# Optimization experiments

Measured on AMD Instinct MI355X. Metric: run time of the kernel, lower is better.

## Reference

```python
import jax, jax.numpy as jnp
import numpy as np

EPS_NORM = 1e-9   # l2_norm eps in original
EPS_ENT = 1e-15   # PyG dense_diff_pool entropy eps


def _sage_block(x, adj, Wl, bl, Wr):
    """SAGEConv(aggr='mean') + ReLU + row L2-norm.
    x: [b,N,din], adj: [b,N,N] binary (adj[i,j]=1 means edge i->j).
    PyG mean-aggr for target j = mean over sources i: (A^T x)/max(deg_in,1).
    out = lin_l(aggr) + lin_r(x); lin_l has bias, lin_r does not.
    """
    deg = jnp.sum(adj, axis=1)                                  # [b,N] in-degree of targets
    agg = jnp.einsum('bij,bid->bjd', adj, x) / jnp.maximum(deg, 1.0)[..., None]
    h = jnp.einsum('bnd,od->bno', agg, Wl) + bl + jnp.einsum('bnd,od->bno', x, Wr)
    h = jax.nn.relu(h)
    return h / (jnp.linalg.norm(h, axis=-1, keepdims=True) + EPS_NORM)


def setup_inputs() -> dict:
    key = jax.random.key(0)
    ks = jax.random.split(key, 16)
    b, N, din, dh, K = 8, 2048, 128, 128, 128
    x = jax.random.normal(ks[0], (b, N, din), dtype=jnp.float32)
    # binary adjacency, avg in-degree ~ 0.01*N ~ 20
    adj = (jax.random.uniform(ks[1], (b, N, N)) < 0.01).astype(jnp.float32)

    def lin(k, o, i):
        return (jax.random.normal(k, (o, i), dtype=jnp.float32) / np.sqrt(i)).astype(jnp.float32)

    return {
        'x': x, 'adj': adj,
        'We1l': lin(ks[2], dh, din), 'be1': jnp.zeros((dh,), jnp.float32), 'We1r': lin(ks[3], dh, din),
        'We2l': lin(ks[4], dh, dh),  'be2': jnp.zeros((dh,), jnp.float32), 'We2r': lin(ks[5], dh, dh),
        'Wa1l': lin(ks[6], dh, din), 'ba1': jnp.zeros((dh,), jnp.float32), 'Wa1r': lin(ks[7], dh, din),
        'Wa2l': lin(ks[8], K, dh),   'ba2': jnp.zeros((K,), jnp.float32), 'Wa2r': lin(ks[9], K, dh),
    }


def reference(x, adj, We1l, be1, We1r, We2l, be2, We2r, Wa1l, ba1, Wa1r, Wa2l, ba2, Wa2r):
    # embedding GNN
    h = _sage_block(x, adj, We1l, be1, We1r)
    h_emb = _sage_block(h, adj, We2l, be2, We2r)          # [b,N,dh]
    # assignment GNN
    a = _sage_block(x, adj, Wa1l, ba1, Wa1r)
    a = _sage_block(a, adj, Wa2l, ba2, Wa2r)              # [b,N,K]
    S = jax.nn.softmax(a, axis=-1)                        # [b,N,K]
    # dense_diff_pool
    h_pooled = jnp.einsum('bnk,bnd->bkd', S, h_emb)       # [b,K,dh]
    adj_pooled = jnp.einsum('bnk,bnm,bml->bkl', S, adj, S)  # [b,K,K]
    link = adj - jnp.einsum('bnk,bmk->bnm', S, S)
    link_loss = jnp.linalg.norm(link) / adj.size          # global Frobenius / numel
    ent_loss = jnp.mean(jnp.sum(-S * jnp.log(S + EPS_ENT), axis=-1))
    return h_pooled, adj_pooled, link_loss, ent_loss
```

## Files before the change

### kernel.cpp

```cpp
#include <hip/hip_runtime.h>
#include <hip/hip_bf16.h>
#include <math.h>

#define BB 8
#define NN 2048
#define DD 128
#define SPL 8
#define CAPH 16

typedef __bf16 bf16x8 __attribute__((ext_vector_type(8)));
typedef float f32x4 __attribute__((ext_vector_type(4)));

__device__ inline unsigned short f2bu(float f) {
  __hip_bfloat16 h = __float2bfloat16(f);
  return *reinterpret_cast<unsigned short*>(&h);
}
__device__ inline unsigned int pack2(float a, float b) {
  return (unsigned int)f2bu(a) | ((unsigned int)f2bu(b) << 16);
}
__device__ inline float blo(unsigned u) { return __uint_as_float(u << 16); }
__device__ inline float bhi(unsigned u) { return __uint_as_float(u & 0xffff0000u); }

__global__ __launch_bounds__(256) void k_build(const float* __restrict__ adj,
                                               const float* __restrict__ x,
                                               unsigned short* __restrict__ colidx,
                                               float* __restrict__ cnth,
                                               float* __restrict__ nnzpart,
                                               __hip_bfloat16* __restrict__ xb) {
  __shared__ float T[2][64][65];
  __shared__ unsigned short L[64][4][CAPH];
  __shared__ int cnts[64][4];
  __shared__ float tsum[64];
  int b = blockIdx.y, j0 = blockIdx.x * 64, z = blockIdx.z;
  int linear = (z * 8 + blockIdx.y) * 32 + blockIdx.x;
  const float* A = adj + (size_t)b * NN * NN + (size_t)z * 1024 * NN + j0;
  int t = threadIdx.x;
  int lr = t >> 2, lc0 = (t & 3) * 16;
  int sc = t & 63, sq = t >> 6;
  float4 pre[4];
  #pragma unroll
  for (int e = 0; e < 4; ++e)
    pre[e] = *(const float4*)(A + (size_t)lr * NN + lc0 + e * 4);
  #pragma unroll
  for (int e = 0; e < 4; ++e)
    *(float4*)&T[0][lr][lc0 + e * 4] = pre[e];
  __syncthreads();
  int cnt = 0;
  for (int ch = 0; ch < 16; ++ch) {
    if (ch + 1 < 16) {
      const float* src = A + (size_t)(ch + 1) * 64 * NN;
      #pragma unroll
      for (int e = 0; e < 4; ++e)
        pre[e] = *(const float4*)(src + (size_t)lr * NN + lc0 + e * 4);
    }
    #pragma unroll
    for (int p = 0; p < 16; ++p) {
      int il = sq * 16 + p;
      float v = T[ch & 1][il][sc];
      if (v != 0.f) {
        L[sc][sq][cnt < CAPH ? cnt : CAPH - 1] = (unsigned short)(z * 1024 + ch * 64 + il);
        ++cnt;
      }
    }
    if (ch + 1 < 16) {
      #pragma unroll
      for (int e = 0; e < 4; ++e)
        *(float4*)&T[(ch + 1) & 1][lr][lc0 + e * 4] = pre[e];
    }
    __syncthreads();
  }
  cnts[sc][sq] = cnt;
  __syncthreads();
  int c = t >> 2, seg = t & 3;
  int n0 = cnts[c][0], n1 = cnts[c][1], n2 = cnts[c][2], n3 = cnts[c][3];
  int tot = n0 + n1 + n2 + n3;
  unsigned short vals[8];
  #pragma unroll
  for (int e = 0; e < 8; ++e) {
    int k = seg * 8 + e;
    unsigned short xv = 0;
    if (k < n0) xv = L[c][0][k];
    else if (k < n0 + n1) xv = L[c][1][k - n0];
    else if (k < n0 + n1 + n2) xv = L[c][2][k - n0 - n1];
    else if (k < tot) xv = L[c][3][k - n0 - n1 - n2];
    vals[e] = xv;
  }
  size_t jg = (size_t)b * NN + j0 + c;
  *(uint4*)(colidx + jg * 64 + z * 32 + seg * 8) = *(uint4*)vals;
  if (seg == 0) {
    cnth[(size_t)z * (BB * NN) + jg] = (float)tot;
    tsum[c] = (float)tot;
  }
  __syncthreads();
  if (t < 64) {
    float s = tsum[t];
    #pragma unroll
    for (int off = 32; off > 0; off >>= 1) s += __shfl_xor(s, off);
    if (t == 0) nnzpart[linear] = s;
  }
  if (z == 0) {
    size_t base = (size_t)(blockIdx.y * 32 + blockIdx.x) * 8192;
    #pragma unroll
    for (int e = 0; e < 8; ++e) {
      size_t off = base + e * 1024 + t * 4;
      float4 a = *(const float4*)(x + off);
      unsigned r2[2] = {pack2(a.x, a.y), pack2(a.z, a.w)};
      *(uint2*)((unsigned short*)xb + off) = *(uint2*)r2;
    }
  }
}

__global__ __launch_bounds__(256) void k_agg(const __hip_bfloat16* __restrict__ V,
                                             const unsigned short* __restrict__ colidx,
                                             const float* __restrict__ cnth,
                                             __hip_bfloat16* __restrict__ out) {
  int w = threadIdx.x >> 6, l = threadIdx.x & 63;
  size_t jg = (size_t)blockIdx.x * 4 + w;
  int b = (int)(jg >> 11);
  int c0 = min((int)cnth[jg], 32);
  int c1 = min((int)cnth[(size_t)BB * NN + jg], 32);
  float sc = 1.f / fmaxf((float)(c0 + c1), 1.f);
  int myi = colidx[jg * 64 + l];
  const unsigned short* Vb = (const unsigned short*)V + (((size_t)b << 11)) * DD;
  float ax = 0.f, ay = 0.f;
  #pragma unroll
  for (int sgm = 0; sgm < 2; ++sgm) {
    int cc = sgm ? c1 : c0;
    int lb = sgm ? 32 : 0;
    int k = 0;
    for (; k + 4 <= cc; k += 4) {
      int i0 = __shfl(myi, lb + k), i1 = __shfl(myi, lb + k + 1);
      int i2 = __shfl(myi, lb + k + 2), i3 = __shfl(myi, lb + k + 3);
      unsigned u0 = *(const unsigned*)(Vb + (size_t)i0 * DD + 2 * l);
      unsigned u1 = *(const unsigned*)(Vb + (size_t)i1 * DD + 2 * l);
      unsigned u2 = *(const unsigned*)(Vb + (size_t)i2 * DD + 2 * l);
      unsigned u3 = *(const unsigned*)(Vb + (size_t)i3 * DD + 2 * l);
      ax += blo(u0) + blo(u1) + blo(u2) + blo(u3);
      ay += bhi(u0) + bhi(u1) + bhi(u2) + bhi(u3);
    }
    for (; k < cc; ++k) {
      int i0 = __shfl(myi, lb + k);
      unsigned u0 = *(const unsigned*)(Vb + (size_t)i0 * DD + 2 * l);
      ax += blo(u0); ay += bhi(u0);
    }
  }
  *(unsigned*)((unsigned short*)out + jg * DD + 2 * l) = pack2(ax * sc, ay * sc);
}

__global__ __launch_bounds__(256) void k_agg2(const __hip_bfloat16* __restrict__ V1,
                                              const __hip_bfloat16* __restrict__ V2,
                                              const unsigned short* __restrict__ colidx,
                                              const float* __restrict__ cnth,
                                              __hip_bfloat16* __restrict__ out1,
                                              __hip_bfloat16* __restrict__ out2) {
  int w = threadIdx.x >> 6, l = threadIdx.x & 63;
  size_t jg = (size_t)blockIdx.x * 4 + w;
  int b = (int)(jg >> 11);
  int c0 = min((int)cnth[jg], 32);
  int c1 = min((int)cnth[(size_t)BB * NN + jg], 32);
  float sc = 1.f / fmaxf((float)(c0 + c1), 1.f);
  int myi = colidx[jg * 64 + l];
  size_t base = (((size_t)b << 11)) * DD + 2 * l;
  const unsigned short* Va = (const unsigned short*)V1 + base;
  const unsigned short* Vb = (const unsigned short*)V2 + base;
  float ax = 0.f, ay = 0.f, bx = 0.f, by = 0.f;
  #pragma unroll
  for (int sgm = 0; sgm < 2; ++sgm) {
    int cc = sgm ? c1 : c0;
    int lb = sgm ? 32 : 0;
    int k = 0;
    for (; k + 2 <= cc; k += 2) {
      int i0 = __shfl(myi, lb + k), i1 = __shfl(myi, lb + k + 1);
      unsigned a0 = *(const unsigned*)(Va + (size_t)i0 * DD);
      unsigned a1 = *(const unsigned*)(Va + (size_t)i1 * DD);
      unsigned b0 = *(const unsigned*)(Vb + (size_t)i0 * DD);
      unsigned b1 = *(const unsigned*)(Vb + (size_t)i1 * DD);
      ax += blo(a0) + blo(a1); ay += bhi(a0) + bhi(a1);
      bx += blo(b0) + blo(b1); by += bhi(b0) + bhi(b1);
    }
    if (k < cc) {
      int i0 = __shfl(myi, lb + k);
      unsigned a0 = *(const unsigned*)(Va + (size_t)i0 * DD);
      unsigned b0 = *(const unsigned*)(Vb + (size_t)i0 * DD);
      ax += blo(a0); ay += bhi(a0);
      bx += blo(b0); by += bhi(b0);
    }
  }
  *(unsigned*)((unsigned short*)out1 + jg * DD + 2 * l) = pack2(ax * sc, ay * sc);
  *(unsigned*)((unsigned short*)out2 + jg * DD + 2 * l) = pack2(bx * sc, by * sc);
}

__global__ __launch_bounds__(256) void k_aggT(const __hip_bfloat16* __restrict__ Sbf,
                                              const unsigned short* __restrict__ colidx,
                                              const float* __restrict__ cnth,
                                              __hip_bfloat16* __restrict__ PT) {
  __shared__ float Lt[128][17];
  int w = threadIdx.x >> 6, l = threadIdx.x & 63;
  size_t jbase = (size_t)blockIdx.x * 16;
  int b = (int)(jbase >> 11);
  const unsigned short* Vb = (const unsigned short*)Sbf + (((size_t)b << 11)) * DD;
  #pragma unroll
  for (int cc4 = 0; cc4 < 4; ++cc4) {
    int jl = w * 4 + cc4;
    size_t jg = jbase + jl;
    int c0 = min((int)cnth[jg], 32);
    int c1 = min((int)cnth[(size_t)BB * NN + jg], 32);
    int myi = colidx[jg * 64 + l];
    float ax = 0.f, ay = 0.f;
    #pragma unroll
    for (int sgm = 0; sgm < 2; ++sgm) {
      int cc = sgm ? c1 : c0;
      int lb = sgm ? 32 : 0;
      int k = 0;
      for (; k + 4 <= cc; k += 4) {
        int i0 = __shfl(myi, lb + k), i1 = __shfl(myi, lb + k + 1);
        int i2 = __shfl(myi, lb + k + 2), i3 = __shfl(myi, lb + k + 3);
        unsigned u0 = *(const unsigned*)(Vb + (size_t)i0 * DD + 2 * l);
        unsigned u1 = *(const unsigned*)(Vb + (size_t)i1 * DD + 2 * l);
        unsigned u2 = *(const unsigned*)(Vb + (size_t)i2 * DD + 2 * l);
        unsigned u3 = *(const unsigned*)(Vb + (size_t)i3 * DD + 2 * l);
        ax += blo(u0) + blo(u1) + blo(u2) + blo(u3);
        ay += bhi(u0) + bhi(u1) + bhi(u2) + bhi(u3);
      }
      for (; k < cc; ++k) {
        int i0 = __shfl(myi, lb + k);
        unsigned u0 = *(const unsigned*)(Vb + (size_t)i0 * DD + 2 * l);
        ax += blo(u0); ay += bhi(u0);
      }
    }
    Lt[2 * l][jl] = ax;
    Lt[2 * l + 1][jl] = ay;
  }
  __syncthreads();
  int t = threadIdx.x;
  if (t < 128) {
    int j0 = (int)(jbase & (NN - 1));
    unsigned wv[8];
    #pragma unroll
    for (int e = 0; e < 8; ++e)
      wv[e] = pack2(Lt[t][2 * e], Lt[t][2 * e + 1]);
    unsigned short* dst = (unsigned short*)PT + ((size_t)b * DD + t) * NN + j0;
    *(uint4*)dst = *(uint4*)&wv[0];
    *(uint4*)(dst + 8) = *(uint4*)&wv[4];
  }
}

__global__ __launch_bounds__(256) void k_lin2(const __hip_bfloat16* __restrict__ AGG,
                                              const __hip_bfloat16* __restrict__ X2,
                                              const float* __restrict__ W0a,
                                              const float* __restrict__ W0b,
                                              const float* __restrict__ b0,
                                              const float* __restrict__ W1a,
                                              const float* __restrict__ W1b,
                                              const float* __restrict__ b1,
                                              __hip_bfloat16* __restrict__ out0,
                                              __hip_bfloat16* __restrict__ out1) {
  __shared__ __align__(16) char smem[64 * 136 * 2 * 2];
  __shared__ __align__(16) __hip_bfloat16 Wsm[2][128 * 72];
  __shared__ float bsm[2][128];
  __hip_bfloat16* As = (__hip_bfloat16*)smem;
  __hip_bfloat16* Xs = As + 64 * 136;
  float* Ho = (float*)smem;

  int b = blockIdx.y, j0 = blockIdx.x * 64;
  int t = threadIdx.x;
  size_t rowbase = (size_t)b * NN + j0;

  if (t < 128) { bsm[0][t] = b0[t]; bsm[1][t] = b1[t]; }
  #pragma unroll
  for (int e = 0; e < 8; ++e) {
    int idx = t + e * 256;
    int r = idx >> 5, c4 = idx & 31;
    size_t g = (rowbase + r) * DD + c4 * 4;
    *(uint2*)&As[r * 136 + c4 * 4] = *(const uint2*)((const unsigned short*)AGG + g);
    *(uint2*)&Xs[r * 136 + c4 * 4] = *(const uint2*)((const unsigned short*)X2 + g);
  }
  __syncthreads();

  int w = t >> 6, l = t & 63;
  int lm = l & 15, lq = l >> 4;
  int jloc = w * 16 + lm;
  f32x4 acc0[8], acc1[8];
  #pragma unroll
  for (int mt = 0; mt < 8; ++mt)
    #pragma unroll
    for (int r = 0; r < 4; ++r) { acc0[mt][r] = 0.f; acc1[mt][r] = 0.f; }

  #pragma unroll
  for (int ph = 0; ph < 2; ++ph) {
    const __hip_bfloat16* Xt = ph ? Xs : As;
    const float* Wx = ph ? W0b : W0a;
    const float* Wy = ph ? W1b : W1a;
    #pragma unroll
    for (int ch = 0; ch < 2; ++ch) {
      __syncthreads();
      #pragma unroll
      for (int e = 0; e < 8; ++e) {
        int idx = t + e * 256;
        int o = idx >> 4, k4 = idx & 15;
        float4 wv = *(const float4*)(Wx + o * DD + ch * 64 + k4 * 4);
        uint2 pw; pw.x = pack2(wv.x, wv.y); pw.y = pack2(wv.z, wv.w);
        *(uint2*)&Wsm[0][o * 72 + k4 * 4] = pw;
        float4 wv2 = *(const float4*)(Wy + o * DD + ch * 64 + k4 * 4);
        uint2 pw2; pw2.x = pack2(wv2.x, wv2.y); pw2.y = pack2(wv2.z, wv2.w);
        *(uint2*)&Wsm[1][o * 72 + k4 * 4] = pw2;
      }
      __syncthreads();
      #pragma unroll
      for (int s = 0; s < 2; ++s) {
        int kx = ch * 64 + s * 32 + lq * 8;
        bf16x8 bfr = *(const bf16x8*)&Xt[jloc * 136 + kx];
        int kw = s * 32 + lq * 8;
        #pragma unroll
        for (int mt = 0; mt < 8; ++mt) {
          bf16x8 a0 = *(const bf16x8*)&Wsm[0][(mt * 16 + lm) * 72 + kw];
          acc0[mt] = __builtin_amdgcn_mfma_f32_16x16x32_bf16(a0, bfr, acc0[mt], 0, 0, 0);
          bf16x8 a1 = *(const bf16x8*)&Wsm[1][(mt * 16 + lm) * 72 + kw];
          acc1[mt] = __builtin_amdgcn_mfma_f32_16x16x32_bf16(a1, bfr, acc1[mt], 0, 0, 0);
        }
      }
    }
  }

  #pragma unroll
  for (int set = 0; set < 2; ++set) {
    __syncthreads();
    f32x4* acc = set ? acc1 : acc0;
    float psum = 0.f;
    float hv[8][4];
    #pragma unroll
    for (int mt = 0; mt < 8; ++mt)
      #pragma unroll
      for (int r = 0; r < 4; ++r) {
        int o = mt * 16 + lq * 4 + r;
        float v = fmaxf(acc[mt][r] + bsm[set][o], 0.f);
        hv[mt][r] = v;
        psum += v * v;
      }
    psum += __shfl_xor(psum, 16);
    psum += __shfl_xor(psum, 32);
    float rn = 1.f / (sqrtf(psum) + 1e-9f);
    #pragma unroll
    for (int mt = 0; mt < 8; ++mt)
      #pragma unroll
      for (int r = 0; r < 4; ++r) {
        int o = mt * 16 + lq * 4 + r;
        Ho[jloc * 132 + o] = hv[mt][r] * rn;
      }
    __syncthreads();
    __hip_bfloat16* ob = set ? out1 : out0;
    #pragma unroll
    for (int e = 0; e < 4; ++e) {
      int idx = t + e * 256;
      int r = idx >> 4, c8 = idx & 15;
      const float* h = &Ho[r * 132 + c8 * 8];
      unsigned pk[4] = {pack2(h[0], h[1]), pack2(h[2], h[3]),
                        pack2(h[4], h[5]), pack2(h[6], h[7])};
      *(uint4*)((unsigned short*)ob + (rowbase + r) * DD + c8 * 8) = *(uint4*)pk;
    }
  }
}

__global__ __launch_bounds__(256) void k_linz(const __hip_bfloat16* __restrict__ AG0,
                                              const __hip_bfloat16* __restrict__ X0,
                                              const float* __restrict__ W0a,
                                              const float* __restrict__ W0b,
                                              const float* __restrict__ b0,
                                              __hip_bfloat16* __restrict__ Sbf,
                                              __hip_bfloat16* __restrict__ STt,
                                              float* __restrict__ entpart,
                                              const __hip_bfloat16* __restrict__ AG1,
                                              const __hip_bfloat16* __restrict__ X1,
                                              const float* __restrict__ W1a,
                                              const float* __restrict__ W1b,
                                              const float* __restrict__ b1,
                                              __hip_bfloat16* __restrict__ out1T) {
  __shared__ __align__(16) char smem[64 * 136 * 2 * 2];
  __shared__ __align__(16) __hip_bfloat16 Wsm[128 * 72];
  __shared__ float bsm[128];
  __shared__ float entred[64];
  __hip_bfloat16* As = (__hip_bfloat16*)smem;
  __hip_bfloat16* Xs = As + 64 * 136;
  float* Ho = (float*)smem;

  int mode = blockIdx.z;
  const __hip_bfloat16* AGG = mode ? AG1 : AG0;
  const __hip_bfloat16* X2 = mode ? X1 : X0;
  const float* Wl = mode ? W1a : W0a;
  const float* Wr = mode ? W1b : W0b;
  const float* bias = mode ? b1 : b0;

  int b = blockIdx.y, j0 = blockIdx.x * 64;
  int t = threadIdx.x;
  size_t rowbase = (size_t)b * NN + j0;

  if (t < 128) bsm[t] = bias[t];
  #pragma unroll
  for (int e = 0; e < 8; ++e) {
    int idx = t + e * 256;
    int r = idx >> 5, c4 = idx & 31;
    size_t g = (rowbase + r) * DD + c4 * 4;
    *(uint2*)&As[r * 136 + c4 * 4] = *(const uint2*)((const unsigned short*)AGG + g);
    *(uint2*)&Xs[r * 136 + c4 * 4] = *(const uint2*)((const unsigned short*)X2 + g);
  }
  __syncthreads();

  int w = t >> 6, l = t & 63;
  int lm = l & 15, lq = l >> 4;
  int jloc = w * 16 + lm;
  f32x4 acc[8];
  #pragma unroll
  for (int mt = 0; mt < 8; ++mt)
    #pragma unroll
    for (int r = 0; r < 4; ++r) acc[mt][r] = 0.f;

  #pragma unroll
  for (int ph = 0; ph < 2; ++ph) {
    const __hip_bfloat16* Xt = ph ? Xs : As;
    const float* W = ph ? Wr : Wl;
    #pragma unroll
    for (int ch = 0; ch < 2; ++ch) {
      __syncthreads();
      #pragma unroll
      for (int e = 0; e < 8; ++e) {
        int idx = t + e * 256;
        int o = idx >> 4, k4 = idx & 15;
        float4 wv = *(const float4*)(W + o * DD + ch * 64 + k4 * 4);
        uint2 pw; pw.x = pack2(wv.x, wv.y); pw.y = pack2(wv.z, wv.w);
        *(uint2*)&Wsm[o * 72 + k4 * 4] = pw;
      }
      __syncthreads();
      #pragma unroll
      for (int s = 0; s < 2; ++s) {
        int kx = ch * 64 + s * 32 + lq * 8;
        bf16x8 bfr = *(const bf16x8*)&Xt[jloc * 136 + kx];
        int kw = s * 32 + lq * 8;
        #pragma unroll
        for (int mt = 0; mt < 8; ++mt) {
          bf16x8 afr = *(const bf16x8*)&Wsm[(mt * 16 + lm) * 72 + kw];
          acc[mt] = __builtin_amdgcn_mfma_f32_16x16x32_bf16(afr, bfr, acc[mt], 0, 0, 0);
        }
      }
    }
  }

  __syncthreads();
  float hv[8][4];
  float psum = 0.f;
  #pragma unroll
  for (int mt = 0; mt < 8; ++mt)
    #pragma unroll
    for (int r = 0; r < 4; ++r) {
      int o = mt * 16 + lq * 4 + r;
      float v = fmaxf(acc[mt][r] + bsm[o], 0.f);
      hv[mt][r] = v;
      psum += v * v;
    }
  psum += __shfl_xor(psum, 16);
  psum += __shfl_xor(psum, 32);
  float rn = 1.f / (sqrtf(psum) + 1e-9f);

  if (mode == 0) {
    float av[8][4];
    float m = -3.4e38f;
    #pragma unroll
    for (int mt = 0; mt < 8; ++mt)
      #pragma unroll
      for (int r = 0; r < 4; ++r) {
        float a = hv[mt][r] * rn;
        av[mt][r] = a;
        m = fmaxf(m, a);
      }
    m = fmaxf(m, __shfl_xor(m, 16));
    m = fmaxf(m, __shfl_xor(m, 32));
    float sum = 0.f;
    #pragma unroll
    for (int mt = 0; mt < 8; ++mt)
      #pragma unroll
      for (int r = 0; r < 4; ++r) {
        float e = expf(av[mt][r] - m);
        av[mt][r] = e;
        sum += e;
      }
    sum += __shfl_xor(sum, 16);
    sum += __shfl_xor(sum, 32);
    float inv = 1.f / sum;
    float ent = 0.f;
    #pragma unroll
    for (int mt = 0; mt < 8; ++mt)
      #pragma unroll
      for (int r = 0; r < 4; ++r) {
        float p = av[mt][r] * inv;
        ent -= p * logf(p + 1e-15f);
        int o = mt * 16 + lq * 4 + r;
        Ho[jloc * 132 + o] = p;
      }
    ent += __shfl_xor(ent, 16);
    ent += __shfl_xor(ent, 32);
    if (l < 16) entred[w * 16 + lm] = ent;
    __syncthreads();
    #pragma unroll
    for (int e = 0; e < 4; ++e) {
      int idx = t + e * 256;
      int r = idx >> 4, c8 = idx & 15;
      const float* h = &Ho[r * 132 + c8 * 8];
      unsigned pk[4] = {pack2(h[0], h[1]), pack2(h[2], h[3]),
                        pack2(h[4], h[5]), pack2(h[6], h[7])};
      *(uint4*)((unsigned short*)Sbf + (rowbase + r) * DD + c8 * 8) = *(uint4*)pk;
    }
    {
      int d = t >> 1, half = t & 1;
      unsigned wv[16];
      #pragma unroll
      for (int e = 0; e < 16; ++e)
        wv[e] = pack2(Ho[(half * 32 + 2 * e) * 132 + d], Ho[(half * 32 + 2 * e + 1) * 132 + d]);
      unsigned short* dst = (unsigned short*)STt + ((size_t)b * DD + d) * NN + j0 + half * 32;
      #pragma unroll
      for (int q = 0; q < 4; ++q)
        *(uint4*)(dst + q * 8) = *(uint4*)&wv[q * 4];
    }
    if (t < 64) {
      float s = entred[t];
      #pragma unroll
      for (int off = 32; off > 0; off >>= 1) s += __shfl_xor(s, off);
      if (t == 0) entpart[blockIdx.y * 32 + blockIdx.x] = s;
    }
  } else {
    #pragma unroll
    for (int mt = 0; mt < 8; ++mt)
      #pragma unroll
      for (int r = 0; r < 4; ++r) {
        int o = mt * 16 + lq * 4 + r;
        Ho[jloc * 132 + o] = hv[mt][r] * rn;
      }
    __syncthreads();
    int d = t >> 1, half = t & 1;
    unsigned wv[16];
    #pragma unroll
    for (int e = 0; e < 16; ++e)
      wv[e] = pack2(Ho[(half * 32 + 2 * e) * 132 + d], Ho[(half * 32 + 2 * e + 1) * 132 + d]);
    unsigned short* dst = (unsigned short*)out1T + ((size_t)b * DD + d) * NN + j0 + half * 32;
    #pragma unroll
    for (int q = 0; q < 4; ++q)
      *(uint4*)(dst + q * 8) = *(uint4*)&wv[q * 4];
  }
}

__global__ __launch_bounds__(256) void k_tnm(const __hip_bfloat16* __restrict__ ST,
                                             const __hip_bfloat16* __restrict__ HT,
                                             const __hip_bfloat16* __restrict__ PT,
                                             float* __restrict__ part) {
  __shared__ __align__(16) __hip_bfloat16 As[128 * 64];
  __shared__ __align__(16) __hip_bfloat16 Bs[128 * 64];
  int pb = blockIdx.y;
  int pair = pb >> 3, b = pb & 7;
  const __hip_bfloat16* Xa = (pair == 1) ? PT : ST;
  const __hip_bfloat16* Ya = (pair == 0) ? HT : ST;
  const __hip_bfloat16* Ab = Xa + (size_t)b * DD * NN;
  const __hip_bfloat16* Bb = Ya + (size_t)b * DD * NN;
  int k0 = blockIdx.x * (NN / SPL);
  int tid = threadIdx.x;
  int w = tid >> 6, l = tid & 63;
  int wj = w & 1, wd = w >> 1;
  int sr = l >> 3, ss = l & 7;
  int lm = l & 15, lq = l >> 4;
  f32x4 acc[4][4];
  #pragma unroll
  for (int a = 0; a < 4; ++a)
    #pragma unroll
    for (int c = 0; c < 4; ++c)
      #pragma unroll
      for (int r = 0; r < 4; ++r) acc[a][c][r] = 0.f;

  for (int kb = 0; kb < (NN / SPL) / 64; ++kb) {
    int kbase = k0 + kb * 64;
    __syncthreads();
    #pragma unroll
    for (int e = 0; e < 4; ++e) {
      int r = 32 * w + 8 * e + sr;
      int g = ss ^ (r & 7);
      const __hip_bfloat16* srcA = Ab + (size_t)r * NN + kbase + g * 8;
      __builtin_amdgcn_global_load_lds(
          (const __attribute__((address_space(1))) void*)srcA,
          (__attribute__((address_space(3))) void*)&As[(32 * w + 8 * e) * 64], 16, 0, 0);
      const __hip_bfloat16* srcB = Bb + (size_t)r * NN + kbase + g * 8;
      __builtin_amdgcn_global_load_lds(
          (const __attribute__((address_space(1))) void*)srcB,
          (__attribute__((address_space(3))) void*)&Bs[(32 * w + 8 * e) * 64], 16, 0, 0);
    }
    __syncthreads();
    #pragma unroll
    for (int ks = 0; ks < 2; ++ks) {
      bf16x8 afr[4], bfr[4];
      int kg = ks * 4 + lq;
      #pragma unroll
      for (int jt = 0; jt < 4; ++jt) {
        int jl = wj * 64 + jt * 16 + lm;
        afr[jt] = *(const bf16x8*)&As[jl * 64 + ((kg ^ (jl & 7)) << 3)];
      }
      #pragma unroll
      for (int dt = 0; dt < 4; ++dt) {
        int dl = wd * 64 + dt * 16 + lm;
        bfr[dt] = *(const bf16x8*)&Bs[dl * 64 + ((kg ^ (dl & 7)) << 3)];
      }
      #pragma unroll
      for (int jt = 0; jt < 4; ++jt)
        #pragma unroll
        for (int dt = 0; dt < 4; ++dt)
          acc[jt][dt] = __builtin_amdgcn_mfma_f32_16x16x32_bf16(afr[jt], bfr[dt], acc[jt][dt], 0, 0, 0);
    }
  }
  float* P = part + ((size_t)(pair * SPL + blockIdx.x) * BB + b) * DD * DD;
  #pragma unroll
  for (int jt = 0; jt < 4; ++jt)
    #pragma unroll
    for (int reg = 0; reg < 4; ++reg) {
      int j = wj * 64 + jt * 16 + lq * 4 + reg;
      float* row = P + (size_t)j * DD;
      #pragma unroll
      for (int dt = 0; dt < 4; ++dt)
        row[wd * 64 + dt * 16 + lm] = acc[jt][dt][reg];
    }
}

__global__ __launch_bounds__(256) void k_tnred3(const float* __restrict__ part,
                                                float* __restrict__ out,
                                                float* __restrict__ trpart,
                                                float* __restrict__ sqpart) {
  __shared__ float red[256];
  int pair = blockIdx.y;
  size_t i = (size_t)blockIdx.x * 256 + threadIdx.x;
  float s = 0.f;
  #pragma unroll
  for (int ks = 0; ks < SPL; ++ks)
    s += part[((size_t)pair * SPL + ks) * (BB * DD * DD) + i];
  float contrib = 0.f;
  if (pair == 0) {
    out[i] = s;
  } else if (pair == 1) {
    out[(size_t)BB * DD * DD + i] = s;
    int rc = (int)(i & (DD * DD - 1));
    if ((rc >> 7) == (rc & 127)) contrib = s;
  } else {
    contrib = s * s;
  }
  red[threadIdx.x] = contrib;
  __syncthreads();
  for (int off = 128; off > 0; off >>= 1) {
    if (threadIdx.x < off) red[threadIdx.x] += red[threadIdx.x + off];
    __syncthreads();
  }
  if (threadIdx.x == 0) {
    if (pair == 1) trpart[blockIdx.x] = red[0];
    else if (pair == 2) sqpart[blockIdx.x] = red[0];
  }
}

__global__ __launch_bounds__(256) void k_final(const float* __restrict__ nnzpart,
                                               const float* __restrict__ entpart,
                                               const float* __restrict__ trpart,
                                               const float* __restrict__ sqpart,
                                               float* __restrict__ out) {
  __shared__ float4 red[256];
  int t = threadIdx.x;
  float4 v;
  v.x = nnzpart[t] + nnzpart[t + 256];
  v.y = entpart[t];
  v.z = trpart[t] + trpart[t + 256];
  v.w = sqpart[t] + sqpart[t + 256];
  red[t] = v;
  __syncthreads();
  for (int off = 128; off > 0; off >>= 1) {
    if (t < off) {
      red[t].x += red[t + off].x; red[t].y += red[t + off].y;
      red[t].z += red[t + off].z; red[t].w += red[t + off].w;
    }
    __syncthreads();
  }
  if (t == 0) {
    double link2 = (double)red[0].x - 2.0 * (double)red[0].z + (double)red[0].w;
    if (link2 < 0.0) link2 = 0.0;
    out[2 * BB * DD * DD]     = (float)(sqrt(link2) / (double)((size_t)BB * NN * NN));
    out[2 * BB * DD * DD + 1] = (float)((double)red[0].y / (double)(BB * NN));
  }
}

extern "C" void kernel_launch(void* const* d_in, const int* in_sizes, int n_in,
                              void* d_out, int out_size, void* d_ws, size_t ws_size,
                              hipStream_t stream) {
  const float* x    = (const float*)d_in[0];
  const float* adj  = (const float*)d_in[1];
  const float* We1l = (const float*)d_in[2];
  const float* be1  = (const float*)d_in[3];
  const float* We1r = (const float*)d_in[4];
  const float* We2l = (const float*)d_in[5];
  const float* be2  = (const float*)d_in[6];
  const float* We2r = (const float*)d_in[7];
  const float* Wa1l = (const float*)d_in[8];
  const float* ba1  = (const float*)d_in[9];
  const float* Wa1r = (const float*)d_in[10];
  const float* Wa2l = (const float*)d_in[11];
  const float* ba2  = (const float*)d_in[12];
  const float* Wa2r = (const float*)d_in[13];
  float* out = (float*)d_out;

  const size_t MB = 1 << 20;
  char* ws = (char*)d_ws;
  float* nnzpart = (float*)(ws);
  float* entpart = (float*)(ws + 4096);
  float* trpart  = (float*)(ws + 8192);
  float* sqpart  = (float*)(ws + 12288);
  float* cnth    = (float*)(ws + 16384);
  unsigned short* colidx = (unsigned short*)(ws + 1 * MB);
  __hip_bfloat16* xbf   = (__hip_bfloat16*)(ws + 3 * MB);
  __hip_bfloat16* agg1  = (__hip_bfloat16*)(ws + 7 * MB);
  __hip_bfloat16* agg2h = (__hip_bfloat16*)(ws + 11 * MB);
  __hip_bfloat16* a1bf  = (__hip_bfloat16*)(ws + 15 * MB);
  __hip_bfloat16* h1bf  = (__hip_bfloat16*)(ws + 19 * MB);
  __hip_bfloat16* Sbf   = (__hip_bfloat16*)(ws + 23 * MB);
  __hip_bfloat16* STt   = (__hip_bfloat16*)(ws + 27 * MB);
  __hip_bfloat16* h2T   = (__hip_bfloat16*)(ws + 31 * MB);
  __hip_bfloat16* PT    = (__hip_bfloat16*)(ws + 35 * MB);
  float* part           = (float*)(ws + 39 * MB);

  dim3 gb(32, 8, 2), glr(32, 8), glz(32, 8, 2), gtm(SPL, 24), gtr(512, 3);

  k_build<<<gb, 256, 0, stream>>>(adj, x, colidx, cnth, nnzpart, xbf);
  k_agg<<<4096, 256, 0, stream>>>(xbf, colidx, cnth, agg1);
  k_lin2<<<glr, 256, 0, stream>>>(agg1, xbf, We1l, We1r, be1, Wa1l, Wa1r, ba1, h1bf, a1bf);
  k_agg2<<<4096, 256, 0, stream>>>(a1bf, h1bf, colidx, cnth, agg1, agg2h);
  k_linz<<<glz, 256, 0, stream>>>(agg1, a1bf, Wa2l, Wa2r, ba2, Sbf, STt, entpart,
                                  agg2h, h1bf, We2l, We2r, be2, h2T);
  k_aggT<<<1024, 256, 0, stream>>>(Sbf, colidx, cnth, PT);
  k_tnm<<<gtm, 256, 0, stream>>>(STt, h2T, PT, part);
  k_tnred3<<<gtr, 256, 0, stream>>>(part, out, trpart, sqpart);
  k_final<<<1, 256, 0, stream>>>(nnzpart, entpart, trpart, sqpart, out);
}
```

Baseline: 312.0 us.

## Fuse neighbor aggregation into linear kernels and fold final reduction via last-block counter

The standalone mean-aggregation kernels are removed. The sparse neighbor gather now runs inside k_lin2 and k_linz, writing aggregated rows straight into shared memory before the MFMA step, which saves a global write and read of the aggregated tensors and two launches. The final scalar reduction is merged into the tensor-reduction kernel using an atomic counter, so the last block finishes it. The trade-off is lower parallelism for the gather (fewer blocks, each wave handling 16 rows serially) and extra memory fences.

```diff
diff --git a/kernel.cpp b/kernel.cpp
--- a/kernel.cpp
+++ b/kernel.cpp
@@ -26,13 +26,15 @@
                                                unsigned short* __restrict__ colidx,
                                                float* __restrict__ cnth,
                                                float* __restrict__ nnzpart,
-                                               __hip_bfloat16* __restrict__ xb) {
+                                               __hip_bfloat16* __restrict__ xb,
+                                               unsigned* __restrict__ counter) {
   __shared__ float T[2][64][65];
   __shared__ unsigned short L[64][4][CAPH];
   __shared__ int cnts[64][4];
   __shared__ float tsum[64];
   int b = blockIdx.y, j0 = blockIdx.x * 64, z = blockIdx.z;
   int linear = (z * 8 + blockIdx.y) * 32 + blockIdx.x;
+  if (linear == 0 && threadIdx.x == 0) *counter = 0;
   const float* A = adj + (size_t)b * NN * NN + (size_t)z * 1024 * NN + j0;
   int t = threadIdx.x;
   int lr = t >> 2, lc0 = (t & 3) * 16;
@@ -110,143 +112,50 @@
   }
 }
 
-__global__ __launch_bounds__(256) void k_agg(const __hip_bfloat16* __restrict__ V,
-                                             const unsigned short* __restrict__ colidx,
-                                             const float* __restrict__ cnth,
-                                             __hip_bfloat16* __restrict__ out) {
-  int w = threadIdx.x >> 6, l = threadIdx.x & 63;
-  size_t jg = (size_t)blockIdx.x * 4 + w;
-  int b = (int)(jg >> 11);
-  int c0 = min((int)cnth[jg], 32);
-  int c1 = min((int)cnth[(size_t)BB * NN + jg], 32);
-  float sc = 1.f / fmaxf((float)(c0 + c1), 1.f);
-  int myi = colidx[jg * 64 + l];
-  const unsigned short* Vb = (const unsigned short*)V + (((size_t)b << 11)) * DD;
-  float ax = 0.f, ay = 0.f;
+__device__ __forceinline__ void gather2(const unsigned short* __restrict__ Vb,
+                                        const unsigned short* __restrict__ colidx,
+                                        const float* __restrict__ cnth,
+                                        size_t gA, size_t gB, int l,
+                                        unsigned& pa, unsigned& pb) {
+  int a0 = min((int)cnth[gA], 32), a1 = min((int)cnth[(size_t)BB * NN + gA], 32);
+  int b0 = min((int)cnth[gB], 32), b1 = min((int)cnth[(size_t)BB * NN + gB], 32);
+  float scA = 1.f / fmaxf((float)(a0 + a1), 1.f);
+  float scB = 1.f / fmaxf((float)(b0 + b1), 1.f);
+  int miA = colidx[gA * 64 + l];
+  int miB = colidx[gB * 64 + l];
+  float axA = 0.f, ayA = 0.f, axB = 0.f, ayB = 0.f;
   #pragma unroll
   for (int sgm = 0; sgm < 2; ++sgm) {
-    int cc = sgm ? c1 : c0;
+    int ccA = sgm ? a1 : a0;
+    int ccB = sgm ? b1 : b0;
     int lb = sgm ? 32 : 0;
-    int k = 0;
-    for (; k + 4 <= cc; k += 4) {
-      int i0 = __shfl(myi, lb + k), i1 = __shfl(myi, lb + k + 1);
-      int i2 = __shfl(myi, lb + k + 2), i3 = __shfl(myi, lb + k + 3);
-      unsigned u0 = *(const unsigned*)(Vb + (size_t)i0 * DD + 2 * l);
-      unsigned u1 = *(const unsigned*)(Vb + (size_t)i1 * DD + 2 * l);
-      unsigned u2 = *(const unsigned*)(Vb + (size_t)i2 * DD + 2 * l);
-      unsigned u3 = *(const unsigned*)(Vb + (size_t)i3 * DD + 2 * l);
-      ax += blo(u0) + blo(u1) + blo(u2) + blo(u3);
-      ay += bhi(u0) + bhi(u1) + bhi(u2) + bhi(u3);
-    }
-    for (; k < cc; ++k) {
-      int i0 = __shfl(myi, lb + k);
-      unsigned u0 = *(const unsigned*)(Vb + (size_t)i0 * DD + 2 * l);
-      ax += blo(u0); ay += bhi(u0);
-    }
-  }
-  *(unsigned*)((unsigned short*)out + jg * DD + 2 * l) = pack2(ax * sc, ay * sc);
-}
-
-__global__ __launch_bounds__(256) void k_agg2(const __hip_bfloat16* __restrict__ V1,
-                                              const __hip_bfloat16* __restrict__ V2,
+    int km = max(ccA, ccB);
+    for (int k = 0; k < km; k += 2) {
+      if (k < ccA) {
+        unsigned u = *(const unsigned*)(Vb + (size_t)__shfl(miA, lb + k) * DD + 2 * l);
+        axA += blo(u); ayA += bhi(u);
+      }
+      if (k + 1 < ccA) {
+        unsigned u = *(const unsigned*)(Vb + (size_t)__shfl(miA, lb + k + 1) * DD + 2 * l);
+        axA += blo(u); ayA += bhi(u);
+      }
+      if (k < ccB) {
+        unsigned u = *(const unsigned*)(Vb + (size_t)__shfl(miB, lb + k) * DD + 2 * l);
+        axB += blo(u); ayB += bhi(u);
+      }
+      if (k + 1 < ccB) {
+        unsigned u = *(const unsigned*)(Vb + (size_t)__shfl(miB, lb + k + 1) * DD + 2 * l);
+        axB += blo(u); ayB += bhi(u);
+      }
+    }
+  }
+  pa = pack2(axA * scA, ayA * scA);
+  pb = pack2(axB * scB, ayB * scB);
+}
+
+__global__ __launch_bounds__(256) void k_lin2(const __hip_bfloat16* __restrict__ V,
                                               const unsigned short* __restrict__ colidx,
                                               const float* __restrict__ cnth,
-                                              __hip_bfloat16* __restrict__ out1,
-                                              __hip_bfloat16* __restrict__ out2) {
-  int w = threadIdx.x >> 6, l = threadIdx.x & 63;
-  size_t jg = (size_t)blockIdx.x * 4 + w;
-  int b = (int)(jg >> 11);
-  int c0 = min((int)cnth[jg], 32);
-  int c1 = min((int)cnth[(size_t)BB * NN + jg], 32);
-  float sc = 1.f / fmaxf((float)(c0 + c1), 1.f);
-  int myi = colidx[jg * 64 + l];
-  size_t base = (((size_t)b << 11)) * DD + 2 * l;
-  const unsigned short* Va = (const unsigned short*)V1 + base;
-  const unsigned short* Vb = (const unsigned short*)V2 + base;
-  float ax = 0.f, ay = 0.f, bx = 0.f, by = 0.f;
-  #pragma unroll
-  for (int sgm = 0; sgm < 2; ++sgm) {
-    int cc = sgm ? c1 : c0;
-    int lb = sgm ? 32 : 0;
-    int k = 0;
-    for (; k + 2 <= cc; k += 2) {
-      int i0 = __shfl(myi, lb + k), i1 = __shfl(myi, lb + k + 1);
-      unsigned a0 = *(const unsigned*)(Va + (size_t)i0 * DD);
-      unsigned a1 = *(const unsigned*)(Va + (size_t)i1 * DD);
-      unsigned b0 = *(const unsigned*)(Vb + (size_t)i0 * DD);
-      unsigned b1 = *(const unsigned*)(Vb + (size_t)i1 * DD);
-      ax += blo(a0) + blo(a1); ay += bhi(a0) + bhi(a1);
-      bx += blo(b0) + blo(b1); by += bhi(b0) + bhi(b1);
-    }
-    if (k < cc) {
-      int i0 = __shfl(myi, lb + k);
-      unsigned a0 = *(const unsigned*)(Va + (size_t)i0 * DD);
-      unsigned b0 = *(const unsigned*)(Vb + (size_t)i0 * DD);
-      ax += blo(a0); ay += bhi(a0);
-      bx += blo(b0); by += bhi(b0);
-    }
-  }
-  *(unsigned*)((unsigned short*)out1 + jg * DD + 2 * l) = pack2(ax * sc, ay * sc);
-  *(unsigned*)((unsigned short*)out2 + jg * DD + 2 * l) = pack2(bx * sc, by * sc);
-}
-
-__global__ __launch_bounds__(256) void k_aggT(const __hip_bfloat16* __restrict__ Sbf,
-                                              const unsigned short* __restrict__ colidx,
-                                              const float* __restrict__ cnth,
-                                              __hip_bfloat16* __restrict__ PT) {
-  __shared__ float Lt[128][17];
-  int w = threadIdx.x >> 6, l = threadIdx.x & 63;
-  size_t jbase = (size_t)blockIdx.x * 16;
-  int b = (int)(jbase >> 11);
-  const unsigned short* Vb = (const unsigned short*)Sbf + (((size_t)b << 11)) * DD;
-  #pragma unroll
-  for (int cc4 = 0; cc4 < 4; ++cc4) {
-    int jl = w * 4 + cc4;
-    size_t jg = jbase + jl;
-    int c0 = min((int)cnth[jg], 32);
-    int c1 = min((int)cnth[(size_t)BB * NN + jg], 32);
-    int myi = colidx[jg * 64 + l];
-    float ax = 0.f, ay = 0.f;
-    #pragma unroll
-    for (int sgm = 0; sgm < 2; ++sgm) {
-      int cc = sgm ? c1 : c0;
-      int lb = sgm ? 32 : 0;
-      int k = 0;
-      for (; k + 4 <= cc; k += 4) {
-        int i0 = __shfl(myi, lb + k), i1 = __shfl(myi, lb + k + 1);
-        int i2 = __shfl(myi, lb + k + 2), i3 = __shfl(myi, lb + k + 3);
-        unsigned u0 = *(const unsigned*)(Vb + (size_t)i0 * DD + 2 * l);
-        unsigned u1 = *(const unsigned*)(Vb + (size_t)i1 * DD + 2 * l);
-        unsigned u2 = *(const unsigned*)(Vb + (size_t)i2 * DD + 2 * l);
-        unsigned u3 = *(const unsigned*)(Vb + (size_t)i3 * DD + 2 * l);
-        ax += blo(u0) + blo(u1) + blo(u2) + blo(u3);
-        ay += bhi(u0) + bhi(u1) + bhi(u2) + bhi(u3);
-      }
-      for (; k < cc; ++k) {
-        int i0 = __shfl(myi, lb + k);
-        unsigned u0 = *(const unsigned*)(Vb + (size_t)i0 * DD + 2 * l);
-        ax += blo(u0); ay += bhi(u0);
-      }
-    }
-    Lt[2 * l][jl] = ax;
-    Lt[2 * l + 1][jl] = ay;
-  }
-  __syncthreads();
-  int t = threadIdx.x;
-  if (t < 128) {
-    int j0 = (int)(jbase & (NN - 1));
-    unsigned wv[8];
-    #pragma unroll
-    for (int e = 0; e < 8; ++e)
-      wv[e] = pack2(Lt[t][2 * e], Lt[t][2 * e + 1]);
-    unsigned short* dst = (unsigned short*)PT + ((size_t)b * DD + t) * NN + j0;
-    *(uint4*)dst = *(uint4*)&wv[0];
-    *(uint4*)(dst + 8) = *(uint4*)&wv[4];
-  }
-}
-
-__global__ __launch_bounds__(256) void k_lin2(const __hip_bfloat16* __restrict__ AGG,
-                                              const __hip_bfloat16* __restrict__ X2,
                                               const float* __restrict__ W0a,
                                               const float* __restrict__ W0b,
                                               const float* __restrict__ b0,
@@ -272,12 +181,19 @@
     int idx = t + e * 256;
     int r = idx >> 5, c4 = idx & 31;
     size_t g = (rowbase + r) * DD + c4 * 4;
-    *(uint2*)&As[r * 136 + c4 * 4] = *(const uint2*)((const unsigned short*)AGG + g);
-    *(uint2*)&Xs[r * 136 + c4 * 4] = *(const uint2*)((const unsigned short*)X2 + g);
-  }
-  __syncthreads();
-
+    *(uint2*)&Xs[r * 136 + c4 * 4] = *(const uint2*)((const unsigned short*)V + g);
+  }
   int w = t >> 6, l = t & 63;
+  const unsigned short* Vb = (const unsigned short*)V + (((size_t)b << 11)) * DD;
+  for (int cc = 0; cc < 16; cc += 2) {
+    int jA = w * 16 + cc;
+    unsigned pa, pb;
+    gather2(Vb, colidx, cnth, rowbase + jA, rowbase + jA + 1, l, pa, pb);
+    *(unsigned*)&As[jA * 136 + 2 * l] = pa;
+    *(unsigned*)&As[(jA + 1) * 136 + 2 * l] = pb;
+  }
+  __syncthreads();
+
   int lm = l & 15, lq = l >> 4;
   int jloc = w * 16 + lm;
   f32x4 acc0[8], acc1[8];
@@ -361,20 +277,20 @@
   }
 }
 
-__global__ __launch_bounds__(256) void k_linz(const __hip_bfloat16* __restrict__ AG0,
-                                              const __hip_bfloat16* __restrict__ X0,
+__global__ __launch_bounds__(256) void k_linz(const __hip_bfloat16* __restrict__ V0,
                                               const float* __restrict__ W0a,
                                               const float* __restrict__ W0b,
                                               const float* __restrict__ b0,
                                               __hip_bfloat16* __restrict__ Sbf,
                                               __hip_bfloat16* __restrict__ STt,
                                               float* __restrict__ entpart,
-                                              const __hip_bfloat16* __restrict__ AG1,
-                                              const __hip_bfloat16* __restrict__ X1,
+                                              const __hip_bfloat16* __restrict__ V1,
                                               const float* __restrict__ W1a,
                                               const float* __restrict__ W1b,
                                               const float* __restrict__ b1,
-                                              __hip_bfloat16* __restrict__ out1T) {
+                                              __hip_bfloat16* __restrict__ out1T,
+                                              const unsigned short* __restrict__ colidx,
+                                              const float* __restrict__ cnth) {
   __shared__ __align__(16) char smem[64 * 136 * 2 * 2];
   __shared__ __align__(16) __hip_bfloat16 Wsm[128 * 72];
   __shared__ float bsm[128];
@@ -384,8 +300,7 @@
   float* Ho = (float*)smem;
 
   int mode = blockIdx.z;
-  const __hip_bfloat16* AGG = mode ? AG1 : AG0;
-  const __hip_bfloat16* X2 = mode ? X1 : X0;
+  const __hip_bfloat16* V = mode ? V1 : V0;
   const float* Wl = mode ? W1a : W0a;
   const float* Wr = mode ? W1b : W0b;
   const float* bias = mode ? b1 : b0;
@@ -400,12 +315,19 @@
     int idx = t + e * 256;
     int r = idx >> 5, c4 = idx & 31;
     size_t g = (rowbase + r) * DD + c4 * 4;
-    *(uint2*)&As[r * 136 + c4 * 4] = *(const uint2*)((const unsigned short*)AGG + g);
-    *(uint2*)&Xs[r * 136 + c4 * 4] = *(const uint2*)((const unsigned short*)X2 + g);
-  }
-  __syncthreads();
-
+    *(uint2*)&Xs[r * 136 + c4 * 4] = *(const uint2*)((const unsigned short*)V + g);
+  }
   int w = t >> 6, l = t & 63;
+  const unsigned short* Vb = (const unsigned short*)V + (((size_t)b << 11)) * DD;
+  for (int cc = 0; cc < 16; cc += 2) {
+    int jA = w * 16 + cc;
+    unsigned pa, pb;
+    gather2(Vb, colidx, cnth, rowbase + jA, rowbase + jA + 1, l, pa, pb);
+    *(unsigned*)&As[jA * 136 + 2 * l] = pa;
+    *(unsigned*)&As[(jA + 1) * 136 + 2 * l] = pb;
+  }
+  __syncthreads();
+
   int lm = l & 15, lq = l >> 4;
   int jloc = w * 16 + lm;
   f32x4 acc[8];
@@ -543,6 +465,61 @@
     #pragma unroll
     for (int q = 0; q < 4; ++q)
       *(uint4*)(dst + q * 8) = *(uint4*)&wv[q * 4];
+  }
+}
+
+__global__ __launch_bounds__(256) void k_aggT(const __hip_bfloat16* __restrict__ Sbf,
+                                              const unsigned short* __restrict__ colidx,
+                                              const float* __restrict__ cnth,
+                                              __hip_bfloat16* __restrict__ PT) {
+  __shared__ float Lt[128][17];
+  int w = threadIdx.x >> 6, l = threadIdx.x & 63;
+  size_t jbase = (size_t)blockIdx.x * 16;
+  int b = (int)(jbase >> 11);
+  const unsigned short* Vb = (const unsigned short*)Sbf + (((size_t)b << 11)) * DD;
+  #pragma unroll
+  for (int cc4 = 0; cc4 < 4; ++cc4) {
+    int jl = w * 4 + cc4;
+    size_t jg = jbase + jl;
+    int c0 = min((int)cnth[jg], 32);
+    int c1 = min((int)cnth[(size_t)BB * NN + jg], 32);
+    int myi = colidx[jg * 64 + l];
+    float ax = 0.f, ay = 0.f;
+    #pragma unroll
+    for (int sgm = 0; sgm < 2; ++sgm) {
+      int cc = sgm ? c1 : c0;
+      int lb = sgm ? 32 : 0;
+      int k = 0;
+      for (; k + 4 <= cc; k += 4) {
+        int i0 = __shfl(myi, lb + k), i1 = __shfl(myi, lb + k + 1);
+        int i2 = __shfl(myi, lb + k + 2), i3 = __shfl(myi, lb + k + 3);
+        unsigned u0 = *(const unsigned*)(Vb + (size_t)i0 * DD + 2 * l);
+        unsigned u1 = *(const unsigned*)(Vb + (size_t)i1 * DD + 2 * l);
+        unsigned u2 = *(const unsigned*)(Vb + (size_t)i2 * DD + 2 * l);
+        unsigned u3 = *(const unsigned*)(Vb + (size_t)i3 * DD + 2 * l);
+        ax += blo(u0) + blo(u1) + blo(u2) + blo(u3);
+        ay += bhi(u0) + bhi(u1) + bhi(u2) + bhi(u3);
+      }
+      for (; k < cc; ++k) {
+        int i0 = __shfl(myi, lb + k);
+        unsigned u0 = *(const unsigned*)(Vb + (size_t)i0 * DD + 2 * l);
+        ax += blo(u0); ay += bhi(u0);
+      }
+    }
+    Lt[2 * l][jl] = ax;
+    Lt[2 * l + 1][jl] = ay;
+  }
+  __syncthreads();
+  int t = threadIdx.x;
+  if (t < 128) {
+    int j0 = (int)(jbase & (NN - 1));
+    unsigned wv[8];
+    #pragma unroll
+    for (int e = 0; e < 8; ++e)
+      wv[e] = pack2(Lt[t][2 * e], Lt[t][2 * e + 1]);
+    unsigned short* dst = (unsigned short*)PT + ((size_t)b * DD + t) * NN + j0;
+    *(uint4*)dst = *(uint4*)&wv[0];
+    *(uint4*)(dst + 8) = *(uint4*)&wv[4];
   }
 }
 
@@ -623,10 +600,13 @@
     }
 }
 
-__global__ __launch_bounds__(256) void k_tnred3(const float* __restrict__ part,
-                                                float* __restrict__ out,
-                                                float* __restrict__ trpart,
-                                                float* __restrict__ sqpart) {
+__global__ __launch_bounds__(256) void k_tnred_final(const float* __restrict__ part,
+                                                     float* __restrict__ out,
+                                                     float* __restrict__ trpart,
+                                                     float* __restrict__ sqpart,
+                                                     const float* __restrict__ nnzpart,
+                                                     const float* __restrict__ entpart,
+                                                     unsigned* __restrict__ counter) {
   __shared__ float red[256];
   int pair = blockIdx.y;
   size_t i = (size_t)blockIdx.x * 256 + threadIdx.x;
@@ -654,34 +634,34 @@
     if (pair == 1) trpart[blockIdx.x] = red[0];
     else if (pair == 2) sqpart[blockIdx.x] = red[0];
   }
-}
-
-__global__ __launch_bounds__(256) void k_final(const float* __restrict__ nnzpart,
-                                               const float* __restrict__ entpart,
-                                               const float* __restrict__ trpart,
-                                               const float* __restrict__ sqpart,
-                                               float* __restrict__ out) {
-  __shared__ float4 red[256];
-  int t = threadIdx.x;
-  float4 v;
-  v.x = nnzpart[t] + nnzpart[t + 256];
-  v.y = entpart[t];
-  v.z = trpart[t] + trpart[t + 256];
-  v.w = sqpart[t] + sqpart[t + 256];
-  red[t] = v;
-  __syncthreads();
-  for (int off = 128; off > 0; off >>= 1) {
-    if (t < off) {
-      red[t].x += red[t + off].x; red[t].y += red[t + off].y;
-      red[t].z += red[t + off].z; red[t].w += red[t + off].w;
-    }
-    __syncthreads();
-  }
-  if (t == 0) {
-    double link2 = (double)red[0].x - 2.0 * (double)red[0].z + (double)red[0].w;
-    if (link2 < 0.0) link2 = 0.0;
-    out[2 * BB * DD * DD]     = (float)(sqrt(link2) / (double)((size_t)BB * NN * NN));
-    out[2 * BB * DD * DD + 1] = (float)((double)red[0].y / (double)(BB * NN));
+  __threadfence();
+  __shared__ unsigned last;
+  if (threadIdx.x == 0) last = atomicAdd(counter, 1u);
+  __syncthreads();
+  if (last == 3 * 512 - 1) {
+    __threadfence();
+    int t = threadIdx.x;
+    float4 v;
+    v.x = nnzpart[t] + nnzpart[t + 256];
+    v.y = entpart[t];
+    v.z = trpart[t] + trpart[t + 256];
+    v.w = sqpart[t] + sqpart[t + 256];
+    __shared__ float4 red4[256];
+    red4[t] = v;
+    __syncthreads();
+    for (int off = 128; off > 0; off >>= 1) {
+      if (t < off) {
+        red4[t].x += red4[t + off].x; red4[t].y += red4[t + off].y;
+        red4[t].z += red4[t + off].z; red4[t].w += red4[t + off].w;
+      }
+      __syncthreads();
+    }
+    if (t == 0) {
+      double link2 = (double)red4[0].x - 2.0 * (double)red4[0].z + (double)red4[0].w;
+      if (link2 < 0.0) link2 = 0.0;
+      out[2 * BB * DD * DD]     = (float)(sqrt(link2) / (double)((size_t)BB * NN * NN));
+      out[2 * BB * DD * DD + 1] = (float)((double)red4[0].y / (double)(BB * NN));
+    }
   }
 }
 
@@ -710,29 +690,27 @@
   float* entpart = (float*)(ws + 4096);
   float* trpart  = (float*)(ws + 8192);
   float* sqpart  = (float*)(ws + 12288);
+  unsigned* counter = (unsigned*)(ws + 14336);
   float* cnth    = (float*)(ws + 16384);
   unsigned short* colidx = (unsigned short*)(ws + 1 * MB);
   __hip_bfloat16* xbf   = (__hip_bfloat16*)(ws + 3 * MB);
-  __hip_bfloat16* agg1  = (__hip_bfloat16*)(ws + 7 * MB);
-  __hip_bfloat16* agg2h = (__hip_bfloat16*)(ws + 11 * MB);
-  __hip_bfloat16* a1bf  = (__hip_bfloat16*)(ws + 15 * MB);
-  __hip_bfloat16* h1bf  = (__hip_bfloat16*)(ws + 19 * MB);
-  __hip_bfloat16* Sbf   = (__hip_bfloat16*)(ws + 23 * MB);
-  __hip_bfloat16* STt   = (__hip_bfloat16*)(ws + 27 * MB);
-  __hip_bfloat16* h2T   = (__hip_bfloat16*)(ws + 31 * MB);
-  __hip_bfloat16* PT    = (__hip_bfloat16*)(ws + 35 * MB);
-  float* part           = (float*)(ws + 39 * MB);
+  __hip_bfloat16* a1bf  = (__hip_bfloat16*)(ws + 7 * MB);
+  __hip_bfloat16* h1bf  = (__hip_bfloat16*)(ws + 11 * MB);
+  __hip_bfloat16* Sbf   = (__hip_bfloat16*)(ws + 15 * MB);
+  __hip_bfloat16* STt   = (__hip_bfloat16*)(ws + 19 * MB);
+  __hip_bfloat16* h2T   = (__hip_bfloat16*)(ws + 23 * MB);
+  __hip_bfloat16* PT    = (__hip_bfloat16*)(ws + 27 * MB);
+  float* part           = (float*)(ws + 31 * MB);
 
   dim3 gb(32, 8, 2), glr(32, 8), glz(32, 8, 2), gtm(SPL, 24), gtr(512, 3);
 
-  k_build<<<gb, 256, 0, stream>>>(adj, x, colidx, cnth, nnzpart, xbf);
-  k_agg<<<4096, 256, 0, stream>>>(xbf, colidx, cnth, agg1);
-  k_lin2<<<glr, 256, 0, stream>>>(agg1, xbf, We1l, We1r, be1, Wa1l, Wa1r, ba1, h1bf, a1bf);
-  k_agg2<<<4096, 256, 0, stream>>>(a1bf, h1bf, colidx, cnth, agg1, agg2h);
-  k_linz<<<glz, 256, 0, stream>>>(agg1, a1bf, Wa2l, Wa2r, ba2, Sbf, STt, entpart,
-                                  agg2h, h1bf, We2l, We2r, be2, h2T);
+  k_build<<<gb, 256, 0, stream>>>(adj, x, colidx, cnth, nnzpart, xbf, counter);
+  k_lin2<<<glr, 256, 0, stream>>>(xbf, colidx, cnth, We1l, We1r, be1,
+                                  Wa1l, Wa1r, ba1, h1bf, a1bf);
+  k_linz<<<glz, 256, 0, stream>>>(a1bf, Wa2l, Wa2r, ba2, Sbf, STt, entpart,
+                                  h1bf, We2l, We2r, be2, h2T, colidx, cnth);
   k_aggT<<<1024, 256, 0, stream>>>(Sbf, colidx, cnth, PT);
   k_tnm<<<gtm, 256, 0, stream>>>(STt, h2T, PT, part);
-  k_tnred3<<<gtr, 256, 0, stream>>>(part, out, trpart, sqpart);
-  k_final<<<1, 256, 0, stream>>>(nnzpart, entpart, trpart, sqpart, out);
-}
+  k_tnred_final<<<gtr, 256, 0, stream>>>(part, out, trpart, sqpart,
+                                         nnzpart, entpart, counter);
+}
```

New measurement: 591.6 us. 89.6% more time.
